# Optimization experiments

Hardware: AMD Instinct MI355X
Metric: run time of the kernel (lower is better)

Reference implementation:

```python
import jax, jax.numpy as jnp
import numpy as np

EPS = 1e-6  # module eps (unused in forward math, kept for fidelity)


def _relative_transform(rot_a, trans_a, rot_b, trans_b):
    # rel_rot = R_a @ R_b^T ; rel_trans = t_a - rel_rot @ t_b
    rel_rot = jnp.einsum('bij,bkj->bik', rot_a, rot_b)          # [B,3,3]
    rel_trans = trans_a - jnp.einsum('bij,bj->bi', rel_rot, trans_b)  # [B,3]
    return rel_rot, rel_trans


def setup_inputs() -> dict:
    key = jax.random.key(0)
    ks = jax.random.split(key, 9)
    B, N = 8, 4096
    return {
        'pred_rot': jax.random.normal(ks[0], (B, 3, 3), jnp.float32),
        'pred_trans': jax.random.normal(ks[1], (B, 3), jnp.float32),
        'ctx_hyp_rot': jax.random.normal(ks[2], (B, 3, 3), jnp.float32),
        'ctx_hyp_trans': jax.random.normal(ks[3], (B, 3), jnp.float32),
        'gt_rot': jax.random.normal(ks[4], (B, 3, 3), jnp.float32),
        'gt_trans': jax.random.normal(ks[5], (B, 3), jnp.float32),
        'ctx_gt_rot': jax.random.normal(ks[6], (B, 3, 3), jnp.float32),
        'ctx_gt_trans': jax.random.normal(ks[7], (B, 3), jnp.float32),
        'model_points': jax.random.normal(ks[8], (B, N, 3), jnp.float32),
    }


def reference(pred_rot, pred_trans, ctx_hyp_rot, ctx_hyp_trans,
              gt_rot, gt_trans, ctx_gt_rot, ctx_gt_trans, model_points):
    rel_pred_rot, rel_pred_trans = _relative_transform(pred_rot, pred_trans, ctx_hyp_rot, ctx_hyp_trans)
    rel_gt_rot, rel_gt_trans = _relative_transform(gt_rot, gt_trans, ctx_gt_rot, ctx_gt_trans)

    # pts = P @ R^T + t   -> [B,N,3]
    pts_pred = jnp.einsum('bnj,bij->bni', model_points, rel_pred_rot) + rel_pred_trans[:, None, :]
    pts_gt = jnp.einsum('bnj,bij->bni', model_points, rel_gt_rot) + rel_gt_trans[:, None, :]

    # pairwise euclidean distance [B,N,M]
    sq = (jnp.sum(pts_pred**2, -1)[:, :, None]
          + jnp.sum(pts_gt**2, -1)[:, None, :]
          - 2.0 * jnp.einsum('bnd,bmd->bnm', pts_pred, pts_gt))
    dist = jnp.sqrt(jnp.maximum(sq, 0.0))

    # symmetric chamfer: mean of row-min + mean of col-min, per batch
    loss_geo = jnp.min(dist, axis=2).mean(axis=1) + jnp.min(dist, axis=1).mean(axis=1)  # [B]
    loss_trans = jnp.abs(rel_pred_trans - rel_gt_trans).mean()
    return (loss_geo.mean(), loss_trans)
```

## Files before the change

kernel.cpp:

```cpp
#include <hip/hip_runtime.h>
#include <hip/hip_bf16.h>
#include <math.h>


#define TPB 256
#define RPT 8
#define MC  128
#define RC  (TPB * RPT)

__device__ __forceinline__ unsigned f2ord(float f) {
    unsigned u = __float_as_uint(f);
    return (u & 0x80000000u) ? ~u : (u | 0x80000000u);
}
__device__ __forceinline__ float ord2f(unsigned u) {
    return (u & 0x80000000u) ? __uint_as_float(u & 0x7fffffffu)
                             : __uint_as_float(~u);
}

__device__ __forceinline__ void rel_tf(const float* __restrict__ Ra,
                                       const float* __restrict__ ta,
                                       const float* __restrict__ Rb,
                                       const float* __restrict__ tb,
                                       float* R, float* t) {
#pragma unroll
    for (int i = 0; i < 3; i++)
#pragma unroll
        for (int k = 0; k < 3; k++)
            R[i * 3 + k] = Ra[i * 3 + 0] * Rb[k * 3 + 0]
                         + Ra[i * 3 + 1] * Rb[k * 3 + 1]
                         + Ra[i * 3 + 2] * Rb[k * 3 + 2];
#pragma unroll
    for (int i = 0; i < 3; i++)
        t[i] = ta[i] - (R[i * 3 + 0] * tb[0] + R[i * 3 + 1] * tb[1]
                      + R[i * 3 + 2] * tb[2]);
}

__global__ void k_prep(const float* __restrict__ pred_rot,
                       const float* __restrict__ pred_trans,
                       const float* __restrict__ ctx_hyp_rot,
                       const float* __restrict__ ctx_hyp_trans,
                       const float* __restrict__ gt_rot,
                       const float* __restrict__ gt_trans,
                       const float* __restrict__ ctx_gt_rot,
                       const float* __restrict__ ctx_gt_trans,
                       const float* __restrict__ mp,
                       float4* __restrict__ pts,
                       unsigned* __restrict__ rowmin,
                       float* __restrict__ out, int B, int N) {
    int idx = blockIdx.x * blockDim.x + threadIdx.x;
    if (idx >= B * N) return;
    int b = idx / N;
    float px = mp[idx * 3 + 0], py = mp[idx * 3 + 1], pz = mp[idx * 3 + 2];
    float R[9], t[3];
#pragma unroll
    for (int g = 0; g < 2; g++) {
        if (g == 0)
            rel_tf(pred_rot + b * 9, pred_trans + b * 3,
                   ctx_hyp_rot + b * 9, ctx_hyp_trans + b * 3, R, t);
        else
            rel_tf(gt_rot + b * 9, gt_trans + b * 3,
                   ctx_gt_rot + b * 9, ctx_gt_trans + b * 3, R, t);
        float x = R[0] * px + R[1] * py + R[2] * pz + t[0];
        float y = R[3] * px + R[4] * py + R[5] * pz + t[1];
        float z = R[6] * px + R[7] * py + R[8] * pz + t[2];
        pts[(size_t)g * B * N + idx] = make_float4(x, y, z, x * x + y * y + z * z);
    }
    rowmin[idx] = 0xFFFFFFFFu;
    rowmin[(size_t)B * N + idx] = 0xFFFFFFFFu;
    if (idx == 0) {
        out[0] = 0.0f;
        float lt = 0.0f;
        for (int bb = 0; bb < B; bb++) {
            float Rp[9], tp[3], Rg[9], tg[3];
            rel_tf(pred_rot + bb * 9, pred_trans + bb * 3,
                   ctx_hyp_rot + bb * 9, ctx_hyp_trans + bb * 3, Rp, tp);
            rel_tf(gt_rot + bb * 9, gt_trans + bb * 3,
                   ctx_gt_rot + bb * 9, ctx_gt_trans + bb * 3, Rg, tg);
            lt += fabsf(tp[0] - tg[0]) + fabsf(tp[1] - tg[1]) + fabsf(tp[2] - tg[2]);
        }
        out[1] = lt / (float)(3 * B);
    }
}

__global__ void __launch_bounds__(TPB) k_chamfer(const float4* __restrict__ pts,
                                                 unsigned* __restrict__ rowmin,
                                                 int B, int N) {
    int dir = blockIdx.z;
    int b = blockIdx.y;
    int nMC = N / MC;
    int rc = blockIdx.x / nMC;
    int mc = blockIdx.x % nMC;
    const float4* Ap = pts + ((size_t)dir * B + b) * N;
    const float4* Bp = pts + ((size_t)(1 - dir) * B + b) * N;

    __shared__ float4 sB[MC];
    int tid = threadIdx.x;
    for (int i = tid; i < MC; i += TPB) sB[i] = Bp[mc * MC + i];

    int rowBase = rc * RC;
    float a2x[RPT], a2y[RPT], a2z[RPT], mn[RPT];
#pragma unroll
    for (int r = 0; r < RPT; r++) {
        float4 a = Ap[rowBase + tid + TPB * r];
        a2x[r] = -2.0f * a.x;
        a2y[r] = -2.0f * a.y;
        a2z[r] = -2.0f * a.z;
        mn[r] = INFINITY;
    }
    __syncthreads();

#pragma unroll 4
    for (int m = 0; m < MC; m++) {
        float4 g = sB[m];
#pragma unroll
        for (int r = 0; r < RPT; r++) {
            float p = __builtin_fmaf(a2z[r], g.z, g.w);
            p = __builtin_fmaf(a2y[r], g.y, p);
            p = __builtin_fmaf(a2x[r], g.x, p);
            mn[r] = fminf(mn[r], p);
        }
    }

#pragma unroll
    for (int r = 0; r < RPT; r++) {
        size_t idx = ((size_t)dir * B + b) * N + rowBase + tid + TPB * r;
        atomicMin(&rowmin[idx], f2ord(mn[r]));
    }
}

__global__ void k_finalize(const float4* __restrict__ pts,
                           const unsigned* __restrict__ rowmin,
                           float* __restrict__ out, int B, int N) {
    int total = 2 * B * N;
    float s = 0.0f;
    for (int i = blockIdx.x * blockDim.x + threadIdx.x; i < total;
         i += gridDim.x * blockDim.x) {
        float part = ord2f(rowmin[i]);
        float sq = fmaxf(part + pts[i].w, 0.0f);
        s += sqrtf(sq);
    }
#pragma unroll
    for (int off = 32; off > 0; off >>= 1) s += __shfl_down(s, off, 64);
    __shared__ float red[TPB / 64];
    int wid = threadIdx.x >> 6, lane = threadIdx.x & 63;
    if (lane == 0) red[wid] = s;
    __syncthreads();
    if (threadIdx.x == 0) {
        float t = 0.0f;
#pragma unroll
        for (int w = 0; w < TPB / 64; w++) t += red[w];
        atomicAdd(&out[0], t / (float)(B * N));
    }
}

extern "C" void kernel_launch(void* const* d_in, const int* in_sizes, int n_in,
                              void* d_out, int out_size, void* d_ws, size_t ws_size,
                              hipStream_t stream) {
    const float* pred_rot      = (const float*)d_in[0];
    const float* pred_trans    = (const float*)d_in[1];
    const float* ctx_hyp_rot   = (const float*)d_in[2];
    const float* ctx_hyp_trans = (const float*)d_in[3];
    const float* gt_rot        = (const float*)d_in[4];
    const float* gt_trans      = (const float*)d_in[5];
    const float* ctx_gt_rot    = (const float*)d_in[6];
    const float* ctx_gt_trans  = (const float*)d_in[7];
    const float* model_points  = (const float*)d_in[8];

    int B = in_sizes[0] / 9;
    int N = in_sizes[8] / (3 * B);

    char* ws = (char*)d_ws;
    float4*   pts    = (float4*)ws;
    unsigned* rowmin = (unsigned*)(ws + (size_t)2 * B * N * 16);
    float*    out    = (float*)d_out;

    k_prep<<<(B * N + TPB - 1) / TPB, TPB, 0, stream>>>(
        pred_rot, pred_trans, ctx_hyp_rot, ctx_hyp_trans,
        gt_rot, gt_trans, ctx_gt_rot, ctx_gt_trans,
        model_points, pts, rowmin, out, B, N);

    dim3 grid((N / RC) * (N / MC), B, 2);
    k_chamfer<<<grid, TPB, 0, stream>>>(pts, rowmin, B, N);

    k_finalize<<<128, TPB, 0, stream>>>(pts, rowmin, out, B, N);
}
```

Before: 98.05 us.

## Restructure chamfer to wave-per-row-group with in-kernel min reduction and fused finalize

Each wavefront now owns 16 query rows and has its 64 lanes stride across all N candidate points, loading them straight from global memory instead of staging tiles in shared memory. The per-row minimum is reduced with cross-lane shuffles and the square-root sum is accumulated in the same kernel. This removes the rowmin buffer, its initialisation, the atomicMin traffic and the separate finalize launch. In exchange every wave re-reads the whole point set from global or L2, there is less row-level reuse per loaded point, and 16 shuffle reductions run per wave.

After: 112.5 us. 14.7% more time.

```diff
diff --git a/kernel.cpp b/kernel.cpp
--- a/kernel.cpp
+++ b/kernel.cpp
@@ -4,18 +4,7 @@
 
 
 #define TPB 256
-#define RPT 8
-#define MC  128
-#define RC  (TPB * RPT)
-
-__device__ __forceinline__ unsigned f2ord(float f) {
-    unsigned u = __float_as_uint(f);
-    return (u & 0x80000000u) ? ~u : (u | 0x80000000u);
-}
-__device__ __forceinline__ float ord2f(unsigned u) {
-    return (u & 0x80000000u) ? __uint_as_float(u & 0x7fffffffu)
-                             : __uint_as_float(~u);
-}
+#define RW  16
 
 __device__ __forceinline__ void rel_tf(const float* __restrict__ Ra,
                                        const float* __restrict__ ta,
@@ -45,7 +34,6 @@
                        const float* __restrict__ ctx_gt_trans,
                        const float* __restrict__ mp,
                        float4* __restrict__ pts,
-                       unsigned* __restrict__ rowmin,
                        float* __restrict__ out, int B, int N) {
     int idx = blockIdx.x * blockDim.x + threadIdx.x;
     if (idx >= B * N) return;
@@ -65,8 +53,6 @@
         float z = R[6] * px + R[7] * py + R[8] * pz + t[2];
         pts[(size_t)g * B * N + idx] = make_float4(x, y, z, x * x + y * y + z * z);
     }
-    rowmin[idx] = 0xFFFFFFFFu;
-    rowmin[(size_t)B * N + idx] = 0xFFFFFFFFu;
     if (idx == 0) {
         out[0] = 0.0f;
         float lt = 0.0f;
@@ -82,68 +68,58 @@
     }
 }
 
-__global__ void __launch_bounds__(TPB) k_chamfer(const float4* __restrict__ pts,
-                                                 unsigned* __restrict__ rowmin,
-                                                 int B, int N) {
-    int dir = blockIdx.z;
-    int b = blockIdx.y;
-    int nMC = N / MC;
-    int rc = blockIdx.x / nMC;
-    int mc = blockIdx.x % nMC;
+__global__ void __launch_bounds__(TPB, 4) k_chamfer(
+        const float4* __restrict__ pts, float* __restrict__ out,
+        int B, int N) {
+    const int wave = threadIdx.x >> 6;
+    const int lane = threadIdx.x & 63;
+    const int rowsPerBlock = (TPB / 64) * RW;
+    const int blocksPerB = N / rowsPerBlock;
+    int bid = blockIdx.x;
+    int dir = bid / (B * blocksPerB);
+    int rem = bid % (B * blocksPerB);
+    int b = rem / blocksPerB;
+    int rblk = rem % blocksPerB;
+
     const float4* Ap = pts + ((size_t)dir * B + b) * N;
     const float4* Bp = pts + ((size_t)(1 - dir) * B + b) * N;
+    int rowBase = rblk * rowsPerBlock + wave * RW;
 
-    __shared__ float4 sB[MC];
-    int tid = threadIdx.x;
-    for (int i = tid; i < MC; i += TPB) sB[i] = Bp[mc * MC + i];
-
-    int rowBase = rc * RC;
-    float a2x[RPT], a2y[RPT], a2z[RPT], mn[RPT];
+    float a2x[RW], a2y[RW], a2z[RW], aw[RW], mn[RW];
 #pragma unroll
-    for (int r = 0; r < RPT; r++) {
-        float4 a = Ap[rowBase + tid + TPB * r];
+    for (int r = 0; r < RW; r++) {
+        float4 a = Ap[rowBase + r];
         a2x[r] = -2.0f * a.x;
         a2y[r] = -2.0f * a.y;
         a2z[r] = -2.0f * a.z;
+        aw[r] = a.w;
         mn[r] = INFINITY;
     }
-    __syncthreads();
 
 #pragma unroll 4
-    for (int m = 0; m < MC; m++) {
-        float4 g = sB[m];
+    for (int mm = 0; mm < N; mm += 64) {
+        float4 g = Bp[mm + lane];
 #pragma unroll
-        for (int r = 0; r < RPT; r++) {
-            float p = __builtin_fmaf(a2z[r], g.z, g.w);
+        for (int r = 0; r < RW; r++) {
+            float p = __builtin_fmaf(a2x[r], g.x, g.w);
             p = __builtin_fmaf(a2y[r], g.y, p);
-            p = __builtin_fmaf(a2x[r], g.x, p);
+            p = __builtin_fmaf(a2z[r], g.z, p);
             mn[r] = fminf(mn[r], p);
         }
     }
 
+    float s = 0.0f;
 #pragma unroll
-    for (int r = 0; r < RPT; r++) {
-        size_t idx = ((size_t)dir * B + b) * N + rowBase + tid + TPB * r;
-        atomicMin(&rowmin[idx], f2ord(mn[r]));
+    for (int r = 0; r < RW; r++) {
+        float m = mn[r];
+#pragma unroll
+        for (int off = 32; off > 0; off >>= 1)
+            m = fminf(m, __shfl_xor(m, off, 64));
+        s += sqrtf(fmaxf(m + aw[r], 0.0f));
     }
-}
 
-__global__ void k_finalize(const float4* __restrict__ pts,
-                           const unsigned* __restrict__ rowmin,
-                           float* __restrict__ out, int B, int N) {
-    int total = 2 * B * N;
-    float s = 0.0f;
-    for (int i = blockIdx.x * blockDim.x + threadIdx.x; i < total;
-         i += gridDim.x * blockDim.x) {
-        float part = ord2f(rowmin[i]);
-        float sq = fmaxf(part + pts[i].w, 0.0f);
-        s += sqrtf(sq);
-    }
-#pragma unroll
-    for (int off = 32; off > 0; off >>= 1) s += __shfl_down(s, off, 64);
     __shared__ float red[TPB / 64];
-    int wid = threadIdx.x >> 6, lane = threadIdx.x & 63;
-    if (lane == 0) red[wid] = s;
+    if (lane == 0) red[wave] = s;
     __syncthreads();
     if (threadIdx.x == 0) {
         float t = 0.0f;
@@ -169,18 +145,15 @@
     int B = in_sizes[0] / 9;
     int N = in_sizes[8] / (3 * B);
 
-    char* ws = (char*)d_ws;
-    float4*   pts    = (float4*)ws;
-    unsigned* rowmin = (unsigned*)(ws + (size_t)2 * B * N * 16);
-    float*    out    = (float*)d_out;
+    float4* pts = (float4*)d_ws;
+    float*  out = (float*)d_out;
 
     k_prep<<<(B * N + TPB - 1) / TPB, TPB, 0, stream>>>(
         pred_rot, pred_trans, ctx_hyp_rot, ctx_hyp_trans,
         gt_rot, gt_trans, ctx_gt_rot, ctx_gt_trans,
-        model_points, pts, rowmin, out, B, N);
+        model_points, pts, out, B, N);
 
-    dim3 grid((N / RC) * (N / MC), B, 2);
-    k_chamfer<<<grid, TPB, 0, stream>>>(pts, rowmin, B, N);
-
-    k_finalize<<<128, TPB, 0, stream>>>(pts, rowmin, out, B, N);
+    int rowsPerBlock = (TPB / 64) * RW;
+    int grid = 2 * B * (N / rowsPerBlock);
+    k_chamfer<<<grid, TPB, 0, stream>>>(pts, out, B, N);
 }
```
